# Performance work log

Measured on AMD Instinct MI355X. Metric: run time of the kernel, lower is better.

The kernel has to match this reference:

```python
import jax, jax.numpy as jnp
import numpy as np

B, S, D, K = 8, 4096, 512, 4096
COMMIT = 0.25


def setup_inputs() -> dict:
    key = jax.random.key(0)
    k1, k2, k3, k4 = jax.random.split(key, 4)
    inputs = jax.random.normal(k1, (B, S, D), dtype=jnp.float32)
    # codebook initialized uniform(-1/K, 1/K) as in the torch module
    codebook = jax.random.uniform(k2, (K, D), dtype=jnp.float32, minval=-1.0 / K, maxval=1.0 / K)
    gate_w = jax.random.normal(k3, (D, D), dtype=jnp.float32) * (1.0 / np.sqrt(D))
    gate_b = jax.random.normal(k4, (D,), dtype=jnp.float32) * 0.01
    return {"inputs": inputs, "codebook": codebook, "gate_w": gate_w, "gate_b": gate_b}


def reference(inputs, codebook, gate_w, gate_b):
    d = inputs.shape[-1]
    flat = inputs.reshape(-1, d)  # [N, D]
    # squared L2 distances to all codes: [N, K]
    distances = (jnp.sum(flat * flat, axis=1, keepdims=True)
                 + jnp.sum(codebook * codebook, axis=1)
                 - 2.0 * jnp.matmul(flat, codebook.T))
    idx = jnp.argmin(distances, axis=1)  # [N]
    # one-hot matmul in the original == direct gather
    quantized = jnp.take(codebook, idx, axis=0).reshape(inputs.shape)
    e_latent_loss = jnp.mean((jax.lax.stop_gradient(quantized) - inputs) ** 2)
    q_latent_loss = jnp.mean((quantized - jax.lax.stop_gradient(inputs)) ** 2)
    loss = q_latent_loss + COMMIT * e_latent_loss
    # straight-through estimator
    quantized_st = inputs + jax.lax.stop_gradient(quantized - inputs)
    gate = jax.nn.sigmoid(jnp.matmul(inputs, gate_w.T) + gate_b)
    output = inputs + quantized_st * gate
    return output, loss
```

## Files before the change

### kernel.cpp

```cpp
#include <hip/hip_runtime.h>
#include <hip/hip_bf16.h>

typedef unsigned short u16;
typedef unsigned char u8;
typedef float f32x4 __attribute__((ext_vector_type(4)));

#define NTOK 32768
#define DIM  512
#define KC   4096

__device__ __forceinline__ void gload_lds16(const void* g, void* l) {
  __builtin_amdgcn_global_load_lds(
      (__attribute__((address_space(1))) void*)g,
      (__attribute__((address_space(3))) void*)l,
      16, 0, 0);
}

__global__ void cvt_x(const float* __restrict__ in, u8* __restrict__ q, int n8) {
  int i = blockIdx.x * blockDim.x + threadIdx.x;
  if (i >= n8) return;
  const float4* p = reinterpret_cast<const float4*>(in) + 2 * (size_t)i;
  float4 a = p[0], b = p[1];
  int u0 = __builtin_amdgcn_cvt_pk_fp8_f32(a.x, a.y, 0, false);
  u0     = __builtin_amdgcn_cvt_pk_fp8_f32(a.z, a.w, u0, true);
  int u1 = __builtin_amdgcn_cvt_pk_fp8_f32(b.x, b.y, 0, false);
  u1     = __builtin_amdgcn_cvt_pk_fp8_f32(b.z, b.w, u1, true);
  uint2 w2; w2.x = (unsigned)u0; w2.y = (unsigned)u1;
  int row   = i >> 6;
  int s8l   = i & 63;
  int chunk = s8l >> 3;
  int s8in  = s8l & 7;
  int h     = (row >> 1) & 7;
  size_t dst = (size_t)row * 512 + chunk * 64 + (size_t)(s8in ^ h) * 8;
  *reinterpret_cast<uint2*>(q + dst) = w2;
}

__global__ void cvt_w(const float* __restrict__ w, u8* __restrict__ wq) {
  int k = blockIdx.x;
  int t = threadIdx.x;
  float c0 = w[(size_t)k * DIM + 2 * t] * 16.f;
  float c1 = w[(size_t)k * DIM + 2 * t + 1] * 16.f;
  int pk = __builtin_amdgcn_cvt_pk_fp8_f32(c0, c1, 0, false);
  int h = (k >> 1) & 7;
  size_t dst = (size_t)k * 512 + (t >> 5) * 64
             + (size_t)(((t >> 2) & 7) ^ h) * 8 + (t & 3) * 2;
  *reinterpret_cast<u16*>(wq + dst) = (u16)(pk & 0xffff);
}

__global__ void cvt_codebook(const float* __restrict__ cb, u8* __restrict__ cbq,
                             float* __restrict__ cnorm) {
  int k = blockIdx.x;
  int t = threadIdx.x;
  float c0 = cb[(size_t)k * DIM + 2 * t];
  float c1 = cb[(size_t)k * DIM + 2 * t + 1];
  int pk = __builtin_amdgcn_cvt_pk_fp8_f32(c0 * 4096.f, c1 * 4096.f, 0, false);
  int h = (k >> 1) & 7;
  size_t dst = (size_t)k * 512 + (t >> 5) * 64
             + (size_t)(((t >> 2) & 7) ^ h) * 8 + (t & 3) * 2;
  *reinterpret_cast<u16*>(cbq + dst) = (u16)(pk & 0xffff);
  float s = c0 * c0 + c1 * c1;
#pragma unroll
  for (int m = 1; m < 64; m <<= 1) s += __shfl_xor(s, m, 64);
  __shared__ float w4[4];
  if ((t & 63) == 0) w4[t >> 6] = s;
  __syncthreads();
  if (t == 0) cnorm[k] = w4[0] + w4[1] + w4[2] + w4[3];
}

__global__ __launch_bounds__(512, 4)
void argmin_fp8(const u8* __restrict__ Xq, const u8* __restrict__ Cq,
                const float* __restrict__ cnorm,
                float* __restrict__ pval, int* __restrict__ pidx) {
  __shared__ u8 As[2][128 * 64];
  __shared__ u8 Bs[2][256 * 64];

  const int tid  = threadIdx.x;
  const int lane = tid & 63;
  const int wid  = tid >> 6;
  const int wr   = wid >> 2;
  const int wc   = wid & 3;
  const int bm   = blockIdx.x;
  const int bn   = blockIdx.y;
  const int l15  = lane & 15, l4 = lane >> 4;

  const u8* Xg = Xq + (size_t)(bm * 128) * DIM;
  const u8* Cg = Cq + (size_t)(bn * 256) * DIM;

  auto stage = [&](int buf, int kt) {
    int kk = kt * 64;
    {
      int row = wid * 16 + (lane >> 2);
      gload_lds16(Xg + (size_t)row * DIM + kk + (lane & 3) * 16,
                  (void*)(As[buf] + wid * 1024));
    }
#pragma unroll
    for (int p = 0; p < 2; p++) {
      int row = p * 128 + wid * 16 + (lane >> 2);
      gload_lds16(Cg + (size_t)row * DIM + kk + (lane & 3) * 16,
                  (void*)(Bs[buf] + p * 8192 + wid * 1024));
    }
  };

  auto rd8 = [&](const u8* base, int row, int s8) -> long long {
    int addr = row * 64 + ((s8 ^ ((row >> 1) & 7)) << 3);
    return *reinterpret_cast<const long long*>(base + addr);
  };

  f32x4 acc[4][4];
#pragma unroll
  for (int i = 0; i < 4; i++)
#pragma unroll
    for (int j = 0; j < 4; j++)
#pragma unroll
      for (int r = 0; r < 4; r++) acc[i][j][r] = 0.f;

  stage(0, 0);
  stage(1, 1);
  asm volatile("s_waitcnt vmcnt(3)" ::: "memory");
  __builtin_amdgcn_s_barrier();
  asm volatile("" ::: "memory");

  for (int t = 0; t < 8; ++t) {
    const u8* A  = As[t & 1];
    const u8* Bt = Bs[t & 1];
    long long bfr[4][2];
#pragma unroll
    for (int ni = 0; ni < 4; ni++)
#pragma unroll
      for (int ks = 0; ks < 2; ks++)
        bfr[ni][ks] = rd8(Bt, wc * 64 + ni * 16 + l15, ks * 4 + l4);
#pragma unroll
    for (int mi = 0; mi < 4; mi++) {
      long long af0 = rd8(A, wr * 64 + mi * 16 + l15, l4);
      long long af1 = rd8(A, wr * 64 + mi * 16 + l15, 4 + l4);
      __builtin_amdgcn_s_setprio(1);
#pragma unroll
      for (int ni = 0; ni < 4; ni++) {
        acc[mi][ni] = __builtin_amdgcn_mfma_f32_16x16x32_fp8_fp8(
            af0, bfr[ni][0], acc[mi][ni], 0, 0, 0);
        acc[mi][ni] = __builtin_amdgcn_mfma_f32_16x16x32_fp8_fp8(
            af1, bfr[ni][1], acc[mi][ni], 0, 0, 0);
      }
      __builtin_amdgcn_s_setprio(0);
    }

    asm volatile("" ::: "memory");
    __builtin_amdgcn_s_barrier();
    asm volatile("" ::: "memory");
    if (t + 2 < 8) {
      stage(t & 1, t + 2);
      asm volatile("s_waitcnt vmcnt(3)" ::: "memory");
      __builtin_amdgcn_s_barrier();
      asm volatile("" ::: "memory");
    } else if (t < 7) {
      asm volatile("s_waitcnt vmcnt(0)" ::: "memory");
      __builtin_amdgcn_s_barrier();
      asm volatile("" ::: "memory");
    }
  }

  const float SC = 4.8828125e-4f;
  float* rv = (float*)As;
  int*   ri = (int*)Bs;
  __syncthreads();

#pragma unroll
  for (int mi = 0; mi < 4; mi++) {
#pragma unroll
    for (int r = 0; r < 4; r++) {
      float best = 1e30f;
      int bi = 0;
#pragma unroll
      for (int ni = 0; ni < 4; ni++) {
        int code = bn * 256 + wc * 64 + ni * 16 + l15;
        float v = cnorm[code] - SC * acc[mi][ni][r];
        if (v < best) { best = v; bi = code; }
      }
#pragma unroll
      for (int m = 1; m < 16; m <<= 1) {
        float ov = __shfl_xor(best, m, 64);
        int   oi = __shfl_xor(bi, m, 64);
        if (ov < best) { best = ov; bi = oi; }
      }
      if (l15 == 0) {
        int tok = wr * 64 + mi * 16 + l4 * 4 + r;
        rv[wc * 128 + tok] = best;
        ri[wc * 128 + tok] = bi;
      }
    }
  }
  __syncthreads();
  if (tid < 128) {
    float bv = rv[tid];
    int   bb = ri[tid];
#pragma unroll
    for (int c = 1; c < 4; c++) {
      float v = rv[c * 128 + tid];
      if (v < bv) { bv = v; bb = ri[c * 128 + tid]; }
    }
    size_t g = (size_t)bn * NTOK + bm * 128 + tid;
    pval[g] = bv;
    pidx[g] = bb;
  }
}

__global__ void argmin_reduce(const float* __restrict__ pval, const int* __restrict__ pidx,
                              int* __restrict__ idx) {
  int t = blockIdx.x * 256 + threadIdx.x;
  float best = 1e30f;
  int bi = 0;
  for (int c = 0; c < 16; c++) {
    float v = pval[(size_t)c * NTOK + t];
    if (v < best) { best = v; bi = pidx[(size_t)c * NTOK + t]; }
  }
  idx[t] = bi;
}

__global__ __launch_bounds__(512, 4)
void gate_fp8(const u8* __restrict__ Xq, const u8* __restrict__ Wq,
              const float* __restrict__ X, const float* __restrict__ Cf,
              const float* __restrict__ gb, const int* __restrict__ idx,
              float* __restrict__ out, float* __restrict__ blockSum) {
  __shared__ u8 As[2][128 * 64];
  __shared__ u8 Bs[2][256 * 64];
  __shared__ float bsum[8];

  const int tid  = threadIdx.x;
  const int lane = tid & 63;
  const int wid  = tid >> 6;
  const int wr   = wid >> 2;
  const int wc   = wid & 3;
  const int bm   = blockIdx.x;
  const int bn   = blockIdx.y;
  const int l15  = lane & 15, l4 = lane >> 4;

  const u8* Xg = Xq + (size_t)(bm * 128) * DIM;
  const u8* Wg = Wq + (size_t)(bn * 256) * DIM;

  auto stage = [&](int buf, int kt) {
    int kk = kt * 64;
    {
      int row = wid * 16 + (lane >> 2);
      gload_lds16(Xg + (size_t)row * DIM + kk + (lane & 3) * 16,
                  (void*)(As[buf] + wid * 1024));
    }
#pragma unroll
    for (int p = 0; p < 2; p++) {
      int row = p * 128 + wid * 16 + (lane >> 2);
      gload_lds16(Wg + (size_t)row * DIM + kk + (lane & 3) * 16,
                  (void*)(Bs[buf] + p * 8192 + wid * 1024));
    }
  };

  auto rd8 = [&](const u8* base, int row, int s8) -> long long {
    int addr = row * 64 + ((s8 ^ ((row >> 1) & 7)) << 3);
    return *reinterpret_cast<const long long*>(base + addr);
  };

  f32x4 acc[4][4];
#pragma unroll
  for (int i = 0; i < 4; i++)
#pragma unroll
    for (int j = 0; j < 4; j++)
#pragma unroll
      for (int r = 0; r < 4; r++) acc[i][j][r] = 0.f;

  stage(0, 0);
  stage(1, 1);
  asm volatile("s_waitcnt vmcnt(3)" ::: "memory");
  __builtin_amdgcn_s_barrier();
  asm volatile("" ::: "memory");

  for (int t = 0; t < 8; ++t) {
    const u8* A  = As[t & 1];
    const u8* Bt = Bs[t & 1];
    long long bfr[4][2];
#pragma unroll
    for (int ni = 0; ni < 4; ni++)
#pragma unroll
      for (int ks = 0; ks < 2; ks++)
        bfr[ni][ks] = rd8(Bt, wc * 64 + ni * 16 + l15, ks * 4 + l4);
#pragma unroll
    for (int mi = 0; mi < 4; mi++) {
      long long af0 = rd8(A, wr * 64 + mi * 16 + l15, l4);
      long long af1 = rd8(A, wr * 64 + mi * 16 + l15, 4 + l4);
      __builtin_amdgcn_s_setprio(1);
#pragma unroll
      for (int ni = 0; ni < 4; ni++) {
        acc[mi][ni] = __builtin_amdgcn_mfma_f32_16x16x32_fp8_fp8(
            af0, bfr[ni][0], acc[mi][ni], 0, 0, 0);
        acc[mi][ni] = __builtin_amdgcn_mfma_f32_16x16x32_fp8_fp8(
            af1, bfr[ni][1], acc[mi][ni], 0, 0, 0);
      }
      __builtin_amdgcn_s_setprio(0);
    }

    asm volatile("" ::: "memory");
    __builtin_amdgcn_s_barrier();
    asm volatile("" ::: "memory");
    if (t + 2 < 8) {
      stage(t & 1, t + 2);
      asm volatile("s_waitcnt vmcnt(3)" ::: "memory");
      __builtin_amdgcn_s_barrier();
      asm volatile("" ::: "memory");
    } else if (t < 7) {
      asm volatile("s_waitcnt vmcnt(0)" ::: "memory");
      __builtin_amdgcn_s_barrier();
      asm volatile("" ::: "memory");
    }
  }

  const float SCW = 0.0625f;
  float lsum = 0.f;
#pragma unroll
  for (int mi = 0; mi < 4; mi++) {
#pragma unroll
    for (int r = 0; r < 4; r++) {
      int token = bm * 128 + wr * 64 + mi * 16 + l4 * 4 + r;
      int code = idx[token];
#pragma unroll
      for (int ni = 0; ni < 4; ni++) {
        int col = bn * 256 + wc * 64 + ni * 16 + l15;
        float logit = SCW * acc[mi][ni][r] + gb[col];
        float g = 1.0f / (1.0f + __expf(-logit));
        float q = Cf[(size_t)code * DIM + col];
        float xx = X[(size_t)token * DIM + col];
        out[(size_t)token * DIM + col] = xx + q * g;
        float d = q - xx;
        lsum += d * d;
      }
    }
  }
#pragma unroll
  for (int m = 1; m < 64; m <<= 1) lsum += __shfl_xor(lsum, m, 64);
  if (lane == 0) bsum[wid] = lsum;
  __syncthreads();
  if (tid == 0) {
    float s = 0.f;
#pragma unroll
    for (int i = 0; i < 8; i++) s += bsum[i];
    blockSum[blockIdx.y * gridDim.x + blockIdx.x] = s;
  }
}

__global__ void finalize(const float* __restrict__ blockSum, float* __restrict__ out_loss) {
  int t = threadIdx.x;
  float s = blockSum[t * 2] + blockSum[t * 2 + 1];
#pragma unroll
  for (int m = 1; m < 64; m <<= 1) s += __shfl_xor(s, m, 64);
  __shared__ float w4[4];
  if ((t & 63) == 0) w4[t >> 6] = s;
  __syncthreads();
  if (t == 0) {
    float tot = w4[0] + w4[1] + w4[2] + w4[3];
    out_loss[0] = 1.25f * tot / 16777216.0f;
  }
}

extern "C" void kernel_launch(void* const* d_in, const int* in_sizes, int n_in,
                              void* d_out, int out_size, void* d_ws, size_t ws_size,
                              hipStream_t stream) {
  const float* X  = (const float*)d_in[0];
  const float* CB = (const float*)d_in[1];
  const float* GW = (const float*)d_in[2];
  const float* GB = (const float*)d_in[3];
  float* out = (float*)d_out;

  char* w = (char*)d_ws;
  size_t off = 0;
  auto alloc = [&](size_t bytes) -> void* {
    void* p = w + off;
    off = (off + bytes + 255) & ~(size_t)255;
    return p;
  };
  u8*    Xq    = (u8*) alloc((size_t)NTOK * DIM);
  u8*    Cq    = (u8*) alloc((size_t)KC * DIM);
  u8*    Wq    = (u8*) alloc((size_t)DIM * DIM);
  float* cnorm = (float*)alloc((size_t)KC * 4);
  float* pval  = (float*)alloc((size_t)16 * NTOK * 4);
  int*   pidx  = (int*)alloc((size_t)16 * NTOK * 4);
  int*   idx   = (int*)alloc((size_t)NTOK * 4);
  float* bsums = (float*)alloc((size_t)512 * 4);

  cvt_x<<<8192, 256, 0, stream>>>(X, Xq, NTOK * DIM / 8);
  cvt_w<<<DIM, 256, 0, stream>>>(GW, Wq);
  cvt_codebook<<<KC, 256, 0, stream>>>(CB, Cq, cnorm);
  argmin_fp8<<<dim3(256, 16), 512, 0, stream>>>(Xq, Cq, cnorm, pval, pidx);
  argmin_reduce<<<128, 256, 0, stream>>>(pval, pidx, idx);
  gate_fp8<<<dim3(256, 2), 512, 0, stream>>>(Xq, Wq, X, CB, GB, idx, out, bsums);
  finalize<<<1, 256, 0, stream>>>(bsums, out + (size_t)NTOK * DIM);
}
```

Baseline: 198.9 us.

## Switch fp8 GEMMs to per-row int8 quantization with i8 MFMA

Replaces the fixed-scale fp8 conversion of inputs, codebook and gate weights with per-row absmax int8 quantization, storing per-row scales. Both argmin and gate GEMMs now use the 16x16x64 i8 MFMA with single 16-byte LDS reads instead of two 8-byte reads and two fp8 MFMAs, and drop the XOR swizzle. Epilogues rescale the int32 accumulators by the row and column scales. The aim is fewer MFMA and LDS instructions and better accuracy for argmin. Removing the swizzle may bring LDS bank conflicts, and the conversion kernels do extra reductions.

Result: faster. 189.0 us (-5.0%).

```diff
diff --git a/kernel.cpp b/kernel.cpp
--- a/kernel.cpp
+++ b/kernel.cpp
@@ -4,6 +4,7 @@
 typedef unsigned short u16;
 typedef unsigned char u8;
 typedef float f32x4 __attribute__((ext_vector_type(4)));
+typedef int i32x4 __attribute__((ext_vector_type(4)));
 
 #define NTOK 32768
 #define DIM  512
@@ -16,63 +17,82 @@
       16, 0, 0);
 }
 
-__global__ void cvt_x(const float* __restrict__ in, u8* __restrict__ q, int n8) {
-  int i = blockIdx.x * blockDim.x + threadIdx.x;
-  if (i >= n8) return;
-  const float4* p = reinterpret_cast<const float4*>(in) + 2 * (size_t)i;
-  float4 a = p[0], b = p[1];
-  int u0 = __builtin_amdgcn_cvt_pk_fp8_f32(a.x, a.y, 0, false);
-  u0     = __builtin_amdgcn_cvt_pk_fp8_f32(a.z, a.w, u0, true);
-  int u1 = __builtin_amdgcn_cvt_pk_fp8_f32(b.x, b.y, 0, false);
-  u1     = __builtin_amdgcn_cvt_pk_fp8_f32(b.z, b.w, u1, true);
-  uint2 w2; w2.x = (unsigned)u0; w2.y = (unsigned)u1;
-  int row   = i >> 6;
-  int s8l   = i & 63;
-  int chunk = s8l >> 3;
-  int s8in  = s8l & 7;
-  int h     = (row >> 1) & 7;
-  size_t dst = (size_t)row * 512 + chunk * 64 + (size_t)(s8in ^ h) * 8;
-  *reinterpret_cast<uint2*>(q + dst) = w2;
-}
-
-__global__ void cvt_w(const float* __restrict__ w, u8* __restrict__ wq) {
-  int k = blockIdx.x;
-  int t = threadIdx.x;
-  float c0 = w[(size_t)k * DIM + 2 * t] * 16.f;
-  float c1 = w[(size_t)k * DIM + 2 * t + 1] * 16.f;
-  int pk = __builtin_amdgcn_cvt_pk_fp8_f32(c0, c1, 0, false);
-  int h = (k >> 1) & 7;
-  size_t dst = (size_t)k * 512 + (t >> 5) * 64
-             + (size_t)(((t >> 2) & 7) ^ h) * 8 + (t & 3) * 2;
-  *reinterpret_cast<u16*>(wq + dst) = (u16)(pk & 0xffff);
-}
-
-__global__ void cvt_codebook(const float* __restrict__ cb, u8* __restrict__ cbq,
-                             float* __restrict__ cnorm) {
-  int k = blockIdx.x;
-  int t = threadIdx.x;
-  float c0 = cb[(size_t)k * DIM + 2 * t];
-  float c1 = cb[(size_t)k * DIM + 2 * t + 1];
-  int pk = __builtin_amdgcn_cvt_pk_fp8_f32(c0 * 4096.f, c1 * 4096.f, 0, false);
-  int h = (k >> 1) & 7;
-  size_t dst = (size_t)k * 512 + (t >> 5) * 64
-             + (size_t)(((t >> 2) & 7) ^ h) * 8 + (t & 3) * 2;
-  *reinterpret_cast<u16*>(cbq + dst) = (u16)(pk & 0xffff);
-  float s = c0 * c0 + c1 * c1;
-#pragma unroll
-  for (int m = 1; m < 64; m <<= 1) s += __shfl_xor(s, m, 64);
-  __shared__ float w4[4];
-  if ((t & 63) == 0) w4[t >> 6] = s;
-  __syncthreads();
-  if (t == 0) cnorm[k] = w4[0] + w4[1] + w4[2] + w4[3];
+__device__ __forceinline__ unsigned pk4(float a, float b, float c, float d, float inv) {
+  int b0 = __float2int_rn(a * inv), b1 = __float2int_rn(b * inv);
+  int b2 = __float2int_rn(c * inv), b3 = __float2int_rn(d * inv);
+  return (unsigned)(b0 & 255) | ((unsigned)(b1 & 255) << 8) |
+         ((unsigned)(b2 & 255) << 16) | ((unsigned)(b3 & 255) << 24);
+}
+
+__global__ void cvt_x_i8(const float* __restrict__ in, u8* __restrict__ q,
+                         float* __restrict__ xs) {
+  int row  = blockIdx.x * 4 + (threadIdx.x >> 6);
+  int lane = threadIdx.x & 63;
+  const float* src = in + (size_t)row * DIM + lane * 8;
+  float4 a = *reinterpret_cast<const float4*>(src);
+  float4 b = *reinterpret_cast<const float4*>(src + 4);
+  float m = fmaxf(fmaxf(fmaxf(fabsf(a.x), fabsf(a.y)), fmaxf(fabsf(a.z), fabsf(a.w))),
+                  fmaxf(fmaxf(fabsf(b.x), fabsf(b.y)), fmaxf(fabsf(b.z), fabsf(b.w))));
+#pragma unroll
+  for (int s = 1; s < 64; s <<= 1) m = fmaxf(m, __shfl_xor(m, s, 64));
+  float inv = 127.0f / fmaxf(m, 1e-20f);
+  uint2 w2;
+  w2.x = pk4(a.x, a.y, a.z, a.w, inv);
+  w2.y = pk4(b.x, b.y, b.z, b.w, inv);
+  *reinterpret_cast<uint2*>(q + (size_t)row * DIM + lane * 8) = w2;
+  if (lane == 0) xs[row] = m * (1.0f / 127.0f);
+}
+
+__global__ void cvt_cb_i8(const float* __restrict__ cb, u8* __restrict__ cq,
+                          float* __restrict__ cnorm, float* __restrict__ cs2) {
+  int row  = blockIdx.x * 4 + (threadIdx.x >> 6);
+  int lane = threadIdx.x & 63;
+  const float* src = cb + (size_t)row * DIM + lane * 8;
+  float4 a = *reinterpret_cast<const float4*>(src);
+  float4 b = *reinterpret_cast<const float4*>(src + 4);
+  float m = fmaxf(fmaxf(fmaxf(fabsf(a.x), fabsf(a.y)), fmaxf(fabsf(a.z), fabsf(a.w))),
+                  fmaxf(fmaxf(fabsf(b.x), fabsf(b.y)), fmaxf(fabsf(b.z), fabsf(b.w))));
+  float s = a.x*a.x + a.y*a.y + a.z*a.z + a.w*a.w
+          + b.x*b.x + b.y*b.y + b.z*b.z + b.w*b.w;
+#pragma unroll
+  for (int sh = 1; sh < 64; sh <<= 1) {
+    m = fmaxf(m, __shfl_xor(m, sh, 64));
+    s += __shfl_xor(s, sh, 64);
+  }
+  float inv = 127.0f / fmaxf(m, 1e-20f);
+  uint2 w2;
+  w2.x = pk4(a.x, a.y, a.z, a.w, inv);
+  w2.y = pk4(b.x, b.y, b.z, b.w, inv);
+  *reinterpret_cast<uint2*>(cq + (size_t)row * DIM + lane * 8) = w2;
+  if (lane == 0) { cnorm[row] = s; cs2[row] = 2.0f * m * (1.0f / 127.0f); }
+}
+
+__global__ void cvt_w_i8(const float* __restrict__ w, u8* __restrict__ wq,
+                         float* __restrict__ ws) {
+  int row  = blockIdx.x * 4 + (threadIdx.x >> 6);
+  int lane = threadIdx.x & 63;
+  const float* src = w + (size_t)row * DIM + lane * 8;
+  float4 a = *reinterpret_cast<const float4*>(src);
+  float4 b = *reinterpret_cast<const float4*>(src + 4);
+  float m = fmaxf(fmaxf(fmaxf(fabsf(a.x), fabsf(a.y)), fmaxf(fabsf(a.z), fabsf(a.w))),
+                  fmaxf(fmaxf(fabsf(b.x), fabsf(b.y)), fmaxf(fabsf(b.z), fabsf(b.w))));
+#pragma unroll
+  for (int s = 1; s < 64; s <<= 1) m = fmaxf(m, __shfl_xor(m, s, 64));
+  float inv = 127.0f / fmaxf(m, 1e-20f);
+  uint2 w2;
+  w2.x = pk4(a.x, a.y, a.z, a.w, inv);
+  w2.y = pk4(b.x, b.y, b.z, b.w, inv);
+  *reinterpret_cast<uint2*>(wq + (size_t)row * DIM + lane * 8) = w2;
+  if (lane == 0) ws[row] = m * (1.0f / 127.0f);
 }
 
 __global__ __launch_bounds__(512, 4)
-void argmin_fp8(const u8* __restrict__ Xq, const u8* __restrict__ Cq,
-                const float* __restrict__ cnorm,
-                float* __restrict__ pval, int* __restrict__ pidx) {
-  __shared__ u8 As[2][128 * 64];
-  __shared__ u8 Bs[2][256 * 64];
+void argmin_i8(const u8* __restrict__ Xq, const u8* __restrict__ Cq,
+               const float* __restrict__ cnorm, const float* __restrict__ cs2,
+               const float* __restrict__ xs,
+               float* __restrict__ pval, int* __restrict__ pidx) {
+  __shared__ __align__(16) u8 As[2][128 * 64];
+  __shared__ __align__(16) u8 Bs[2][256 * 64];
 
   const int tid  = threadIdx.x;
   const int lane = tid & 63;
@@ -101,18 +121,17 @@
     }
   };
 
-  auto rd8 = [&](const u8* base, int row, int s8) -> long long {
-    int addr = row * 64 + ((s8 ^ ((row >> 1) & 7)) << 3);
-    return *reinterpret_cast<const long long*>(base + addr);
+  auto rd16 = [&](const u8* base, int row) -> i32x4 {
+    return *reinterpret_cast<const i32x4*>(base + row * 64 + l4 * 16);
   };
 
-  f32x4 acc[4][4];
+  i32x4 acc[4][4];
 #pragma unroll
   for (int i = 0; i < 4; i++)
 #pragma unroll
     for (int j = 0; j < 4; j++)
 #pragma unroll
-      for (int r = 0; r < 4; r++) acc[i][j][r] = 0.f;
+      for (int r = 0; r < 4; r++) acc[i][j][r] = 0;
 
   stage(0, 0);
   stage(1, 1);
@@ -123,24 +142,17 @@
   for (int t = 0; t < 8; ++t) {
     const u8* A  = As[t & 1];
     const u8* Bt = Bs[t & 1];
-    long long bfr[4][2];
-#pragma unroll
-    for (int ni = 0; ni < 4; ni++)
-#pragma unroll
-      for (int ks = 0; ks < 2; ks++)
-        bfr[ni][ks] = rd8(Bt, wc * 64 + ni * 16 + l15, ks * 4 + l4);
+    i32x4 bfr[4];
+#pragma unroll
+    for (int ni = 0; ni < 4; ni++) bfr[ni] = rd16(Bt, wc * 64 + ni * 16 + l15);
 #pragma unroll
     for (int mi = 0; mi < 4; mi++) {
-      long long af0 = rd8(A, wr * 64 + mi * 16 + l15, l4);
-      long long af1 = rd8(A, wr * 64 + mi * 16 + l15, 4 + l4);
+      i32x4 af = rd16(A, wr * 64 + mi * 16 + l15);
       __builtin_amdgcn_s_setprio(1);
 #pragma unroll
-      for (int ni = 0; ni < 4; ni++) {
-        acc[mi][ni] = __builtin_amdgcn_mfma_f32_16x16x32_fp8_fp8(
-            af0, bfr[ni][0], acc[mi][ni], 0, 0, 0);
-        acc[mi][ni] = __builtin_amdgcn_mfma_f32_16x16x32_fp8_fp8(
-            af1, bfr[ni][1], acc[mi][ni], 0, 0, 0);
-      }
+      for (int ni = 0; ni < 4; ni++)
+        acc[mi][ni] = __builtin_amdgcn_mfma_i32_16x16x64_i8(
+            af, bfr[ni], acc[mi][ni], 0, 0, 0);
       __builtin_amdgcn_s_setprio(0);
     }
 
@@ -159,22 +171,31 @@
     }
   }
 
-  const float SC = 4.8828125e-4f;
   float* rv = (float*)As;
   int*   ri = (int*)Bs;
   __syncthreads();
 
+  float cn[4], c2[4];
+  int   cd[4];
+#pragma unroll
+  for (int ni = 0; ni < 4; ni++) {
+    cd[ni] = bn * 256 + wc * 64 + ni * 16 + l15;
+    cn[ni] = cnorm[cd[ni]];
+    c2[ni] = cs2[cd[ni]];
+  }
+
 #pragma unroll
   for (int mi = 0; mi < 4; mi++) {
 #pragma unroll
     for (int r = 0; r < 4; r++) {
+      int token = bm * 128 + wr * 64 + mi * 16 + l4 * 4 + r;
+      float xsv = xs[token];
       float best = 1e30f;
       int bi = 0;
 #pragma unroll
       for (int ni = 0; ni < 4; ni++) {
-        int code = bn * 256 + wc * 64 + ni * 16 + l15;
-        float v = cnorm[code] - SC * acc[mi][ni][r];
-        if (v < best) { best = v; bi = code; }
+        float v = cn[ni] - xsv * c2[ni] * (float)acc[mi][ni][r];
+        if (v < best) { best = v; bi = cd[ni]; }
       }
 #pragma unroll
       for (int m = 1; m < 16; m <<= 1) {
@@ -217,12 +238,13 @@
 }
 
 __global__ __launch_bounds__(512, 4)
-void gate_fp8(const u8* __restrict__ Xq, const u8* __restrict__ Wq,
-              const float* __restrict__ X, const float* __restrict__ Cf,
-              const float* __restrict__ gb, const int* __restrict__ idx,
-              float* __restrict__ out, float* __restrict__ blockSum) {
-  __shared__ u8 As[2][128 * 64];
-  __shared__ u8 Bs[2][256 * 64];
+void gate_i8(const u8* __restrict__ Xq, const u8* __restrict__ Wq,
+             const float* __restrict__ X, const float* __restrict__ Cf,
+             const float* __restrict__ gb, const float* __restrict__ xs,
+             const float* __restrict__ ws, const int* __restrict__ idx,
+             float* __restrict__ out, float* __restrict__ blockSum) {
+  __shared__ __align__(16) u8 As[2][128 * 64];
+  __shared__ __align__(16) u8 Bs[2][256 * 64];
   __shared__ float bsum[8];
 
   const int tid  = threadIdx.x;
@@ -252,18 +274,17 @@
     }
   };
 
-  auto rd8 = [&](const u8* base, int row, int s8) -> long long {
-    int addr = row * 64 + ((s8 ^ ((row >> 1) & 7)) << 3);
-    return *reinterpret_cast<const long long*>(base + addr);
+  auto rd16 = [&](const u8* base, int row) -> i32x4 {
+    return *reinterpret_cast<const i32x4*>(base + row * 64 + l4 * 16);
   };
 
-  f32x4 acc[4][4];
+  i32x4 acc[4][4];
 #pragma unroll
   for (int i = 0; i < 4; i++)
 #pragma unroll
     for (int j = 0; j < 4; j++)
 #pragma unroll
-      for (int r = 0; r < 4; r++) acc[i][j][r] = 0.f;
+      for (int r = 0; r < 4; r++) acc[i][j][r] = 0;
 
   stage(0, 0);
   stage(1, 1);
@@ -274,24 +295,17 @@
   for (int t = 0; t < 8; ++t) {
     const u8* A  = As[t & 1];
     const u8* Bt = Bs[t & 1];
-    long long bfr[4][2];
-#pragma unroll
-    for (int ni = 0; ni < 4; ni++)
-#pragma unroll
-      for (int ks = 0; ks < 2; ks++)
-        bfr[ni][ks] = rd8(Bt, wc * 64 + ni * 16 + l15, ks * 4 + l4);
+    i32x4 bfr[4];
+#pragma unroll
+    for (int ni = 0; ni < 4; ni++) bfr[ni] = rd16(Bt, wc * 64 + ni * 16 + l15);
 #pragma unroll
     for (int mi = 0; mi < 4; mi++) {
-      long long af0 = rd8(A, wr * 64 + mi * 16 + l15, l4);
-      long long af1 = rd8(A, wr * 64 + mi * 16 + l15, 4 + l4);
+      i32x4 af = rd16(A, wr * 64 + mi * 16 + l15);
       __builtin_amdgcn_s_setprio(1);
 #pragma unroll
-      for (int ni = 0; ni < 4; ni++) {
-        acc[mi][ni] = __builtin_amdgcn_mfma_f32_16x16x32_fp8_fp8(
-            af0, bfr[ni][0], acc[mi][ni], 0, 0, 0);
-        acc[mi][ni] = __builtin_amdgcn_mfma_f32_16x16x32_fp8_fp8(
-            af1, bfr[ni][1], acc[mi][ni], 0, 0, 0);
-      }
+      for (int ni = 0; ni < 4; ni++)
+        acc[mi][ni] = __builtin_amdgcn_mfma_i32_16x16x64_i8(
+            af, bfr[ni], acc[mi][ni], 0, 0, 0);
       __builtin_amdgcn_s_setprio(0);
     }
 
@@ -310,7 +324,14 @@
     }
   }
 
-  const float SCW = 0.0625f;
+  float wsv[4], gbv[4];
+  int   cl[4];
+#pragma unroll
+  for (int ni = 0; ni < 4; ni++) {
+    cl[ni] = bn * 256 + wc * 64 + ni * 16 + l15;
+    wsv[ni] = ws[cl[ni]];
+    gbv[ni] = gb[cl[ni]];
+  }
   float lsum = 0.f;
 #pragma unroll
   for (int mi = 0; mi < 4; mi++) {
@@ -318,10 +339,11 @@
     for (int r = 0; r < 4; r++) {
       int token = bm * 128 + wr * 64 + mi * 16 + l4 * 4 + r;
       int code = idx[token];
+      float xsv = xs[token];
 #pragma unroll
       for (int ni = 0; ni < 4; ni++) {
-        int col = bn * 256 + wc * 64 + ni * 16 + l15;
-        float logit = SCW * acc[mi][ni][r] + gb[col];
+        int col = cl[ni];
+        float logit = xsv * wsv[ni] * (float)acc[mi][ni][r] + gbv[ni];
         float g = 1.0f / (1.0f + __expf(-logit));
         float q = Cf[(size_t)code * DIM + col];
         float xx = X[(size_t)token * DIM + col];
@@ -376,17 +398,20 @@
   u8*    Xq    = (u8*) alloc((size_t)NTOK * DIM);
   u8*    Cq    = (u8*) alloc((size_t)KC * DIM);
   u8*    Wq    = (u8*) alloc((size_t)DIM * DIM);
+  float* xsc   = (float*)alloc((size_t)NTOK * 4);
   float* cnorm = (float*)alloc((size_t)KC * 4);
+  float* cs2   = (float*)alloc((size_t)KC * 4);
+  float* wsc   = (float*)alloc((size_t)DIM * 4);
   float* pval  = (float*)alloc((size_t)16 * NTOK * 4);
   int*   pidx  = (int*)alloc((size_t)16 * NTOK * 4);
   int*   idx   = (int*)alloc((size_t)NTOK * 4);
   float* bsums = (float*)alloc((size_t)512 * 4);
 
-  cvt_x<<<8192, 256, 0, stream>>>(X, Xq, NTOK * DIM / 8);
-  cvt_w<<<DIM, 256, 0, stream>>>(GW, Wq);
-  cvt_codebook<<<KC, 256, 0, stream>>>(CB, Cq, cnorm);
-  argmin_fp8<<<dim3(256, 16), 512, 0, stream>>>(Xq, Cq, cnorm, pval, pidx);
+  cvt_x_i8<<<8192, 256, 0, stream>>>(X, Xq, xsc);
+  cvt_cb_i8<<<1024, 256, 0, stream>>>(CB, Cq, cnorm, cs2);
+  cvt_w_i8<<<128, 256, 0, stream>>>(GW, Wq, wsc);
+  argmin_i8<<<dim3(256, 16), 512, 0, stream>>>(Xq, Cq, cnorm, cs2, xsc, pval, pidx);
   argmin_reduce<<<128, 256, 0, stream>>>(pval, pidx, idx);
-  gate_fp8<<<dim3(256, 2), 512, 0, stream>>>(Xq, Wq, X, CB, GB, idx, out, bsums);
+  gate_i8<<<dim3(256, 2), 512, 0, stream>>>(Xq, Wq, X, CB, GB, xsc, wsc, idx, out, bsums);
   finalize<<<1, 256, 0, stream>>>(bsums, out + (size_t)NTOK * DIM);
 }
```
